# Performance work log

Hardware: AMD Instinct MI355X
Metric: run time of the kernel (lower is better)

The kernel has to match this reference:

```python
import jax, jax.numpy as jnp
import numpy as np

H = 1024      # hidden_size
MEL = 128     # mel_bins
B = 32        # batch
TENC = 512    # encoder time steps
TMEL = 400    # decoder (mel) time steps


def setup_inputs() -> dict:
    key = jax.random.key(0)
    ks = jax.random.split(key, 16)
    def w(k, shape, s=0.02):
        return jax.random.normal(k, shape, dtype=jnp.float32) * s
    return dict(
        encoder_hidden=w(ks[0], (4, B, H), 0.1),
        encoder_outputs=w(ks[1], (B, TENC, H), 0.1),
        y=w(ks[2], (B, TMEL, MEL), 1.0),
        mel_spec_lens=jax.random.randint(ks[3], (B,), 1, TMEL),
        # attention linear
        W_attn=w(ks[4], (H, H)), b_attn=jnp.zeros((H,), jnp.float32),
        # GRU layer 0 (input MEL) and layer 1 (input H); gate order r,z,n as in torch
        W_ih0=w(ks[5], (3 * H, MEL)), W_hh0=w(ks[6], (3 * H, H)),
        b_ih0=jnp.zeros((3 * H,), jnp.float32), b_hh0=jnp.zeros((3 * H,), jnp.float32),
        W_ih1=w(ks[7], (3 * H, H)), W_hh1=w(ks[8], (3 * H, H)),
        b_ih1=jnp.zeros((3 * H,), jnp.float32), b_hh1=jnp.zeros((3 * H,), jnp.float32),
        # concat2hidden, mel projection, eos gate
        Wc=w(ks[9], (H, 2 * H)), bc=jnp.zeros((H,), jnp.float32),
        Wp=w(ks[10], (MEL, H)), bp=jnp.zeros((MEL,), jnp.float32),
        Wg=w(ks[11], (1, H)), bg=jnp.zeros((1,), jnp.float32),
    )


def gru_cell(x, h, Wih, Whh, bih, bhh):
    # torch GRUCell math: gates ordered (r, z, n)
    gi = x @ Wih.T + bih          # [B, 3H]
    gh = h @ Whh.T + bhh          # [B, 3H]
    ir, iz, inn = jnp.split(gi, 3, axis=-1)
    hr, hz, hn = jnp.split(gh, 3, axis=-1)
    r = jax.nn.sigmoid(ir + hr)
    z = jax.nn.sigmoid(iz + hz)
    n = jnp.tanh(inn + r * hn)
    return (1.0 - z) * n + z * h


def reference(encoder_hidden, encoder_outputs, y, mel_spec_lens,
              W_attn, b_attn,
              W_ih0, W_hh0, b_ih0, b_hh0,
              W_ih1, W_hh1, b_ih1, b_hh1,
              Wc, bc, Wp, bp, Wg, bg):
    Bsz, Tmel, mel = y.shape
    # attention energy depends only on encoder_outputs -> hoist out of the loop (same math)
    energy = encoder_outputs @ W_attn.T + b_attn          # [B, Te, H]
    h0 = encoder_hidden[0]                                 # decoder_hidden = encoder_hidden[:num_layers]
    h1 = encoder_hidden[1]
    dec_in0 = jnp.zeros((Bsz, mel), y.dtype)               # SOS frame

    def step(carry, _):
        dec_in, h0, h1 = carry
        h0 = gru_cell(dec_in, h0, W_ih0, W_hh0, b_ih0, b_hh0)
        h1 = gru_cell(h0, h1, W_ih1, W_hh1, b_ih1, b_hh1)   # rnn_output = top-layer state [B, H]
        scores = jnp.einsum('bh,bth->bt', h1, energy)       # additive-style dot scores [B, Te]
        probs = jax.nn.softmax(scores, axis=1)
        context = jnp.einsum('bt,bth->bh', probs, encoder_outputs)  # [B, H]
        co = jnp.tanh(jnp.concatenate([h1, context], axis=-1) @ Wc.T + bc)  # [B, H]
        mel_out = co @ Wp.T + bp                            # [B, MEL]
        gate = (co @ Wg.T + bg)[:, 0]                       # [B]
        return (mel_out, h0, h1), (mel_out, gate)

    _, (mels, gates) = jax.lax.scan(step, (dec_in0, h0, h1), None, length=Tmel)
    mels = jnp.transpose(mels, (1, 0, 2))                   # [B, T, MEL]
    gates = gates.T                                          # [B, T]

    t = jnp.arange(Tmel)
    mask = t[None, :] > mel_spec_lens[:, None]               # strictly-greater, as in source
    masked_mel = jnp.where(mask[:, :, None], 0.0, mels)
    masked_gate = jnp.where(mask, 1000.0, gates)
    return masked_mel, masked_gate, mask
```

## Files before the change

### kernel.cpp

```cpp
#include <hip/hip_runtime.h>
#include <stdint.h>
#include <stddef.h>


#define TM  400

typedef unsigned short ushort_t;
typedef short  short8  __attribute__((ext_vector_type(8)));
typedef float  float4v __attribute__((ext_vector_type(4)));

#define DEVI static __device__ __forceinline__

#define SB_IH0  0
#define SB_IH1  393216
#define SB_HH0  3538944
#define SB_HH1  6684672
#define SB_AT   9830400
#define SB_WC   10878976
#define SW_TOT  12976128

__device__ __align__(16) ushort_t g_sw[SW_TOT];
__device__ __align__(16) ushort_t g_h0b[32768], g_h1b[32768];
__device__ __align__(16) float g_h0f[32768], g_h1f[32768];
__device__ __align__(16) float g_ubuf[32768], g_ctxn[32768];
__device__ __align__(16) float g_gh0[98304], g_gh1[98304];
__device__ __align__(16) float g_cbuf[32], g_sden[32];
__device__ __align__(16) float g_melsum[4096], g_gatesum[32];
__device__ __align__(16) float g_pctx[262144];
__device__ __align__(16) float g_pden[256];
__device__ __align__(16) float g_pmel[262144];
__device__ __align__(16) float g_pgate[2048];

DEVI ushort_t f2b(float f) {
  union { float f; uint32_t u; } c; c.f = f;
  uint32_t u = c.u + 0x7fffu + ((c.u >> 16) & 1u);
  return (ushort_t)(u >> 16);
}
DEVI float sigm(float x) { return 1.f / (1.f + __expf(-x)); }

DEVI float4v mfma16(short8 a, short8 b, float4v c) {
  return __builtin_amdgcn_mfma_f32_16x16x32_bf16(a, b, c, 0, 0, 0);
}

DEVI short8 frag_bias(const float* p, const float* bias) {
  short8 r;
#pragma unroll
  for (int i = 0; i < 8; ++i) r[i] = (short)f2b(p[i] + bias[i]);
  return r;
}
DEVI short8 frag_scale(const float* p, float s) {
  short8 r;
#pragma unroll
  for (int i = 0; i < 8; ++i) r[i] = (short)f2b(p[i] * s);
  return r;
}

DEVI float4v gemm_bf16(const ushort_t* Ab, int K, const ushort_t* Bw,
                       int ntile, int mu, int lane) {
  float4v acc = {0.f, 0.f, 0.f, 0.f};
  const int KB = K >> 5;
  const ushort_t* a = Ab + (size_t)(mu * 16 + (lane & 15)) * K + ((lane >> 4) << 3);
  const ushort_t* b = Bw + ((size_t)ntile * KB * 64 + lane) * 8;
  for (int kb = 0; kb < KB; ++kb) {
    short8 av = *(const short8*)(a + kb * 32);
    short8 bv = *(const short8*)(b + (size_t)kb * 512);
    acc = mfma16(av, bv, acc);
  }
  return acc;
}

DEVI float4v gemm_s1(const float* mp, const float* bp, const ushort_t* Bw,
                     int ntile, int mu, int lane) {
  float4v acc = {0.f, 0.f, 0.f, 0.f};
  const int m = mu * 16 + (lane & 15), ko = (lane >> 4) << 3;
  const ushort_t* b = Bw + ((size_t)ntile * 4 * 64 + lane) * 8;
  for (int kb = 0; kb < 4; ++kb) {
    short8 av = frag_bias(mp + m * 128 + kb * 32 + ko, bp + kb * 32 + ko);
    acc = mfma16(av, *(const short8*)(b + (size_t)kb * 512), acc);
  }
  return acc;
}

DEVI float4v gemm_s4(const ushort_t* h1b, const float* ctxn, const float* sden,
                     const ushort_t* Bw, int ntile, int mu, int lane) {
  float4v acc = {0.f, 0.f, 0.f, 0.f};
  const int m = mu * 16 + (lane & 15), ko = (lane >> 4) << 3;
  const ushort_t* a0 = h1b + m * 1024 + ko;
  const float* a1 = ctxn + m * 1024 + ko;
  const float den = sden[m];
  const float inv = (den > 1e-35f) ? (1.f / den) : 0.f;
  const ushort_t* b = Bw + ((size_t)ntile * 64 * 64 + lane) * 8;
  for (int kb = 0; kb < 32; ++kb)
    acc = mfma16(*(const short8*)(a0 + kb * 32), *(const short8*)(b + (size_t)kb * 512), acc);
  for (int kb = 32; kb < 64; ++kb) {
    short8 av = frag_scale(a1 + (kb - 32) * 32, inv);
    acc = mfma16(av, *(const short8*)(b + (size_t)kb * 512), acc);
  }
  return acc;
}

DEVI void put_tile(float* sh, int q, int lane, float4v a) {
  const int base = q * 256 + (lane & 15);
#pragma unroll
  for (int i = 0; i < 4; ++i) sh[base + ((lane >> 4) * 4 + i) * 16] = a[i];
}

__global__ void k_swz(const float* __restrict__ W0, const float* __restrict__ W1,
                      const float* __restrict__ W2, const float* __restrict__ W3,
                      const float* __restrict__ WA, const float* __restrict__ WC) {
  long fid = (long)blockIdx.x * 256 + threadIdx.x;
  if (fid >= 1622016) return;
  const float* src; int N, K; long base, local; bool tr = false;
  if      (fid < 49152)   { src = W0; N = 3072; K = 128;  base = SB_IH0; local = fid; }
  else if (fid < 442368)  { src = W1; N = 3072; K = 1024; base = SB_IH1; local = fid - 49152; }
  else if (fid < 835584)  { src = W2; N = 3072; K = 1024; base = SB_HH0; local = fid - 442368; }
  else if (fid < 1228800) { src = W3; N = 3072; K = 1024; base = SB_HH1; local = fid - 835584; }
  else if (fid < 1359872) { src = WA; N = 1024; K = 1024; base = SB_AT;  local = fid - 1228800; tr = true; }
  else                    { src = WC; N = 1024; K = 2048; base = SB_WC;  local = fid - 1359872; }
  const int L = (int)(local & 63);
  long rest = local >> 6;
  const int KB = K >> 5;
  const int kb = (int)(rest % KB);
  const int nt = (int)(rest / KB);
  const int n  = nt * 16 + (L & 15);
  const int k0 = kb * 32 + ((L >> 4) << 3);
  short8 r;
#pragma unroll
  for (int i = 0; i < 8; ++i) {
    float f = tr ? src[(size_t)(k0 + i) * N + n] : src[(size_t)n * K + (k0 + i)];
    r[i] = (short)f2b(f);
  }
  *(short8*)(g_sw + base + local * 8) = r;
}

__global__ void k_init(const float* __restrict__ ehid, const int* __restrict__ lens,
                       float* __restrict__ out, int out_size) {
  int i = blockIdx.x * 256 + threadIdx.x;
  if (i < 32768) { float v = ehid[i]; g_h0f[i] = v; g_h0b[i] = f2b(v); }
  else if (i < 65536) { int j = i - 32768; float v = ehid[32768 + j]; g_h1f[j] = v; g_h1b[j] = f2b(v); }
  else if (i < 78336) {
    int mi = i - 65536; int b = mi / 400, tt = mi % 400;
    int idx = 1651200 + mi;
    if (idx < out_size)
      out[idx] = (tt > lens[b]) ? 1.0f : 0.0f;
  }
}

__global__ void k_mel() {
  const int wg = blockIdx.x, tid = threadIdx.x;
  if (wg < 16) {
    const int e = wg * 256 + tid;
    float s = 0.f;
    for (int w = 0; w < 64; ++w) s += g_pmel[w * 4096 + e];
    g_melsum[e] = s;
  } else if (tid < 32) {
    float s = 0.f;
    for (int w = 0; w < 64; ++w) s += g_pgate[w * 32 + tid];
    g_gatesum[tid] = s;
  }
}

__global__ void k_s1(int t, const float* __restrict__ b_ih0,
                     const float* __restrict__ bp, const float* __restrict__ bg,
                     const int* __restrict__ lens,
                     float* __restrict__ out, int out_size) {
  const int wg = blockIdx.x, tid = threadIdx.x;
  const int lane = tid & 63, wv = tid >> 6;
  __shared__ __align__(16) float sh[1536];
  if (wg < 64) {
    if (t >= TM) return;
    const int qa = (wv < 2) ? wv * 2 : wv + 2;
    const int qb = (wv < 2) ? wv * 2 + 1 : -1;
    const ushort_t* SW_ih0 = g_sw + SB_IH0;
    float4v acc;
    { int g = qa >> 1, mu = qa & 1;
      acc = (t > 0) ? gemm_s1(g_melsum, bp, SW_ih0, g * 64 + wg, mu, lane)
                    : float4v{0.f, 0.f, 0.f, 0.f};
      put_tile(sh, qa, lane, acc); }
    if (qb >= 0) { int g = qb >> 1, mu = qb & 1;
      acc = (t > 0) ? gemm_s1(g_melsum, bp, SW_ih0, g * 64 + wg, mu, lane)
                    : float4v{0.f, 0.f, 0.f, 0.f};
      put_tile(sh, qb, lane, acc); }
    __syncthreads();
    const int jl = tid & 15, mr = tid >> 4, jg = wg * 16 + jl;
    const float bir = b_ih0[jg], biz = b_ih0[1024 + jg], bin = b_ih0[2048 + jg];
#pragma unroll
    for (int mu = 0; mu < 2; ++mu) {
      const int b = mu * 16 + mr;
      float gr = sh[mu * 256 + tid]       + bir + g_gh0[b * 3072 + jg];
      float gz = sh[(2 + mu) * 256 + tid] + biz + g_gh0[b * 3072 + 1024 + jg];
      float gn = sh[(4 + mu) * 256 + tid] + bin;
      float r = sigm(gr), z = sigm(gz);
      float nn = tanhf(gn + r * g_gh0[b * 3072 + 2048 + jg]);
      float h = (1.f - z) * nn + z * g_h0f[b * 1024 + jg];
      g_h0f[b * 1024 + jg] = h; g_h0b[b * 1024 + jg] = f2b(h);
    }
  } else {
    if (t == 0) return;
    const int fo = (wg - 64) * 256 + tid;
    if (fo < 4096) {
      const int b = fo >> 7, m = fo & 127;
      const bool mk = (t - 1) > lens[b];
      float v = mk ? 0.f : g_melsum[fo] + bp[m];
      int idx = b * 51200 + (t - 1) * 128 + m;
      if (idx < out_size) out[idx] = v;
    } else if (fo < 4128) {
      const int b = fo - 4096;
      const bool mk = (t - 1) > lens[b];
      float g = mk ? 1000.f : g_gatesum[b] + bg[0];
      int idx = 1638400 + b * 400 + (t - 1);
      if (idx < out_size) out[idx] = g;
    }
  }
}

__global__ void k_s2(const float* __restrict__ b_ih1) {
  const int wg = blockIdx.x, tid = threadIdx.x;
  const int lane = tid & 63, wv = tid >> 6;
  __shared__ __align__(16) float sh[1536];
  const int qa = (wv < 2) ? wv * 2 : wv + 2;
  const int qb = (wv < 2) ? wv * 2 + 1 : -1;
  const ushort_t* SW_ih1 = g_sw + SB_IH1;
  { int g = qa >> 1, mu = qa & 1;
    put_tile(sh, qa, lane, gemm_bf16(g_h0b, 1024, SW_ih1, g * 64 + wg, mu, lane)); }
  if (qb >= 0) { int g = qb >> 1, mu = qb & 1;
    put_tile(sh, qb, lane, gemm_bf16(g_h0b, 1024, SW_ih1, g * 64 + wg, mu, lane)); }
  __syncthreads();
  const int jl = tid & 15, mr = tid >> 4, jg = wg * 16 + jl;
  const float bir = b_ih1[jg], biz = b_ih1[1024 + jg], bin = b_ih1[2048 + jg];
#pragma unroll
  for (int mu = 0; mu < 2; ++mu) {
    const int b = mu * 16 + mr;
    float gr = sh[mu * 256 + tid]       + bir + g_gh1[b * 3072 + jg];
    float gz = sh[(2 + mu) * 256 + tid] + biz + g_gh1[b * 3072 + 1024 + jg];
    float gn = sh[(4 + mu) * 256 + tid] + bin;
    float r = sigm(gr), z = sigm(gz);
    float nn = tanhf(gn + r * g_gh1[b * 3072 + 2048 + jg]);
    float h = (1.f - z) * nn + z * g_h1f[b * 1024 + jg];
    g_h1f[b * 1024 + jg] = h; g_h1b[b * 1024 + jg] = f2b(h);
  }
}

__global__ void k_s2b(const float* __restrict__ b_hh0,
                      const float* __restrict__ b_hh1,
                      const float* __restrict__ b_attn) {
  const int wg = blockIdx.x, tid = threadIdx.x;
  const int lane = tid & 63, wv = tid >> 6;
  __shared__ __align__(16) float sh[1536];
  const int qa = (wv < 2) ? wv * 2 : wv + 2;
  const int qb = (wv < 2) ? wv * 2 + 1 : -1;
  if (wg < 128) {
    const ushort_t* Ab = (wg < 64) ? g_h0b : g_h1b;
    const ushort_t* Bw = g_sw + ((wg < 64) ? SB_HH0 : SB_HH1);
    const float* bhh = (wg < 64) ? b_hh0 : b_hh1;
    float* ghb = (wg < 64) ? g_gh0 : g_gh1;
    const int w16 = wg & 63;
    { int g = qa >> 1, mu = qa & 1;
      put_tile(sh, qa, lane, gemm_bf16(Ab, 1024, Bw, g * 64 + w16, mu, lane)); }
    if (qb >= 0) { int g = qb >> 1, mu = qb & 1;
      put_tile(sh, qb, lane, gemm_bf16(Ab, 1024, Bw, g * 64 + w16, mu, lane)); }
    __syncthreads();
    const int jl = tid & 15, mr = tid >> 4, jg = w16 * 16 + jl;
#pragma unroll
    for (int mu = 0; mu < 2; ++mu) {
      const int b = mu * 16 + mr;
#pragma unroll
      for (int g = 0; g < 3; ++g)
        ghb[b * 3072 + g * 1024 + jg] = sh[(g * 2 + mu) * 256 + tid] + bhh[g * 1024 + jg];
    }
  } else if (wg < 192) {
    const int nt = wg - 128;
    if (wv < 2) put_tile(sh, wv, lane, gemm_bf16(g_h1b, 1024, g_sw + SB_AT, nt, wv, lane));
    __syncthreads();
    const int nl = tid & 15, mr = tid >> 4, n = nt * 16 + nl;
    g_ubuf[mr * 1024 + n]        = sh[tid];
    g_ubuf[(16 + mr) * 1024 + n] = sh[256 + tid];
  } else {
    const int b = tid >> 3, seg = tid & 7;
    const float* hp = g_h1f + b * 1024 + seg * 128;
    const float* ba = b_attn + seg * 128;
    float s = 0.f;
    for (int k = 0; k < 128; ++k) s += hp[k] * ba[k];
    for (int off = 1; off < 8; off <<= 1) s += __shfl_xor(s, off, 64);
    if (seg == 0) g_cbuf[b] = s;
  }
}

__global__ void k_s3(const float* __restrict__ enc) {
  const int wg = blockIdx.x, tid = threadIdx.x;
  const int lane = tid & 63, wv = tid >> 6;
  __shared__ __align__(16) float sh[4160];
  const int b = wg >> 3, slot = wg & 7;
  const float* ub = g_ubuf + b * 1024;
  float4v u[4];
#pragma unroll
  for (int c = 0; c < 4; ++c) u[c] = *(const float4v*)(ub + c * 256 + lane * 4);
  const float cb = g_cbuf[b];
  float4v cx[4] = {{0.f,0.f,0.f,0.f},{0.f,0.f,0.f,0.f},{0.f,0.f,0.f,0.f},{0.f,0.f,0.f,0.f}};
  float sw = 0.f;
  const int t0 = slot * 64 + wv * 16;
  for (int it = 0; it < 16; ++it) {
    const float* encp = enc + ((size_t)(b * 512 + t0 + it) * 1024) + lane * 4;
    float4v e[4];
#pragma unroll
    for (int c = 0; c < 4; ++c) e[c] = *(const float4v*)(encp + c * 256);
    float s = 0.f;
#pragma unroll
    for (int c = 0; c < 4; ++c)
#pragma unroll
      for (int j = 0; j < 4; ++j) s += u[c][j] * e[c][j];
    for (int off = 1; off < 64; off <<= 1) s += __shfl_xor(s, off, 64);
    float sc = fminf(fmaxf(s + cb, -70.f), 70.f);
    const float p = __expf(sc);
    sw += p;
#pragma unroll
    for (int c = 0; c < 4; ++c) cx[c] += p * e[c];
  }
#pragma unroll
  for (int c = 0; c < 4; ++c)
    *(float4v*)&sh[wv * 1024 + c * 256 + lane * 4] = cx[c];
  if (lane == 0) sh[4096 + wv] = sw;
  __syncthreads();
  float4v t4 = {0.f, 0.f, 0.f, 0.f};
#pragma unroll
  for (int v = 0; v < 4; ++v) t4 += *(const float4v*)&sh[v * 1024 + tid * 4];
  *(float4v*)&g_pctx[(size_t)(slot * 32 + b) * 1024 + tid * 4] = t4;
  if (tid == 0)
    g_pden[slot * 32 + b] = sh[4096] + sh[4097] + sh[4098] + sh[4099];
}

__global__ void k_red() {
  const int b = blockIdx.x, tid = threadIdx.x;
  float4v t4 = {0.f, 0.f, 0.f, 0.f};
#pragma unroll
  for (int s = 0; s < 8; ++s)
    t4 += *(const float4v*)&g_pctx[(size_t)(s * 32 + b) * 1024 + tid * 4];
  *(float4v*)&g_ctxn[b * 1024 + tid * 4] = t4;
  if (tid == 0) {
    float d = 0.f;
#pragma unroll
    for (int s = 0; s < 8; ++s) d += g_pden[s * 32 + b];
    g_sden[b] = d;
  }
}

__global__ void k_s4(const float* __restrict__ bc, const float* __restrict__ Wp,
                     const float* __restrict__ Wg) {
  const int wg = blockIdx.x, tid = threadIdx.x;
  const int lane = tid & 63, wv = tid >> 6;
  __shared__ __align__(16) float sh[2048];
  if (wv < 2)
    put_tile(sh, wv, lane, gemm_s4(g_h1b, g_ctxn, g_sden, g_sw + SB_WC, wg, wv, lane));
  __syncthreads();
  const int jl = tid & 15, mr = tid >> 4;
  const float bcv = bc[wg * 16 + jl];
#pragma unroll
  for (int mu = 0; mu < 2; ++mu) {
    const int b = mu * 16 + mr;
    sh[1536 + b * 16 + jl] = tanhf(sh[mu * 256 + tid] + bcv);
  }
  __syncthreads();
  const int b2 = tid >> 3, mg = tid & 7;
  const float* cop = &sh[1536 + b2 * 16];
  for (int mm = 0; mm < 16; ++mm) {
    const int m = mg * 16 + mm;
    const float* wp = Wp + m * 1024 + wg * 16;
    float s = 0.f;
#pragma unroll
    for (int j2 = 0; j2 < 16; ++j2) s += wp[j2] * cop[j2];
    g_pmel[wg * 4096 + b2 * 128 + m] = s;
  }
  if (tid < 32) {
    const float* cop2 = &sh[1536 + tid * 16];
    const float* wgp = Wg + wg * 16;
    float g = 0.f;
#pragma unroll
    for (int j2 = 0; j2 < 16; ++j2) g += wgp[j2] * cop2[j2];
    g_pgate[wg * 32 + tid] = g;
  }
}

extern "C" void kernel_launch(void* const* d_in, const int* in_sizes, int n_in,
                              void* d_out, int out_size, void* d_ws, size_t ws_size,
                              hipStream_t stream) {
  const float* ehid  = (const float*)d_in[0];
  const float* enc   = (const float*)d_in[1];
  const int*   lens  = (const int*)d_in[3];
  const float* W_attn= (const float*)d_in[4];
  const float* b_attn= (const float*)d_in[5];
  const float* W_ih0 = (const float*)d_in[6];
  const float* W_hh0 = (const float*)d_in[7];
  const float* b_ih0 = (const float*)d_in[8];
  const float* b_hh0 = (const float*)d_in[9];
  const float* W_ih1 = (const float*)d_in[10];
  const float* W_hh1 = (const float*)d_in[11];
  const float* b_ih1 = (const float*)d_in[12];
  const float* b_hh1 = (const float*)d_in[13];
  const float* Wc    = (const float*)d_in[14];
  const float* bc    = (const float*)d_in[15];
  const float* Wp    = (const float*)d_in[16];
  const float* bp    = (const float*)d_in[17];
  const float* Wg    = (const float*)d_in[18];
  const float* bg    = (const float*)d_in[19];
  float* out = (float*)d_out;

  k_swz<<<6336, 256, 0, stream>>>(W_ih0, W_ih1, W_hh0, W_hh1, W_attn, Wc);
  k_init<<<306, 256, 0, stream>>>(ehid, lens, out, out_size);
  k_s2b<<<193, 256, 0, stream>>>(b_hh0, b_hh1, b_attn);
  for (int t = 0; t < TM; ++t) {
    k_mel<<<17, 256, 0, stream>>>();
    k_s1<<<96, 256, 0, stream>>>(t, b_ih0, bp, bg, lens, out, out_size);
    k_s2<<<64, 256, 0, stream>>>(b_ih1);
    k_s2b<<<193, 256, 0, stream>>>(b_hh0, b_hh1, b_attn);
    k_s3<<<256, 256, 0, stream>>>(enc);
    k_red<<<32, 256, 0, stream>>>();
    k_s4<<<64, 256, 0, stream>>>(bc, Wp, Wg);
  }
  k_mel<<<17, 256, 0, stream>>>();
  k_s1<<<96, 256, 0, stream>>>(TM, b_ih0, bp, bg, lens, out, out_size);
}
```

Before: 25.46 ms.

## Fuse decoder loop into persistent kernel with grid barriers and folded mel projection

Replaces the roughly 2800 per-step kernel launches with one persistent 256-workgroup kernel that runs all 400 timesteps, separated by software grid barriers built on atomics. It also pre-multiplies W_ih0 by Wp, so the layer-0 input GEMM reads the bf16 concat output directly and the mel reduction no longer sits on the critical path. The context partial sums now use float atomics instead of a separate reduction kernel. The risks are barrier latency, a deadlock if not all 256 workgroups are co-resident, atomic contention, and precision changes from the folded weight and nondeterministic summation order.

```diff
diff --git a/kernel.cpp b/kernel.cpp
--- a/kernel.cpp
+++ b/kernel.cpp
@@ -3,7 +3,8 @@
 #include <stddef.h>
 
 
-#define TM  400
+#define TM   400
+#define NWG  256
 
 typedef unsigned short ushort_t;
 typedef short  short8  __attribute__((ext_vector_type(8)));
@@ -11,25 +12,25 @@
 
 #define DEVI static __device__ __forceinline__
 
-#define SB_IH0  0
-#define SB_IH1  393216
-#define SB_HH0  3538944
-#define SB_HH1  6684672
-#define SB_AT   9830400
-#define SB_WC   10878976
-#define SW_TOT  12976128
+#define SB_WF   0
+#define SB_IH1  3145728
+#define SB_HH0  6291456
+#define SB_HH1  9437184
+#define SB_AT   12582912
+#define SB_WC   13631488
+#define SW_TOT  15728640
 
 __device__ __align__(16) ushort_t g_sw[SW_TOT];
+__device__ __align__(16) float    g_wf[3145728];
 __device__ __align__(16) ushort_t g_h0b[32768], g_h1b[32768];
-__device__ __align__(16) float g_h0f[32768], g_h1f[32768];
-__device__ __align__(16) float g_ubuf[32768], g_ctxn[32768];
-__device__ __align__(16) float g_gh0[98304], g_gh1[98304];
-__device__ __align__(16) float g_cbuf[32], g_sden[32];
-__device__ __align__(16) float g_melsum[4096], g_gatesum[32];
-__device__ __align__(16) float g_pctx[262144];
-__device__ __align__(16) float g_pden[256];
-__device__ __align__(16) float g_pmel[262144];
-__device__ __align__(16) float g_pgate[2048];
+__device__ __align__(16) float    g_h0f[32768], g_h1f[32768];
+__device__ __align__(16) float    g_ubuf[32768], g_cbuf[32], g_b0f[3072];
+__device__ __align__(16) float    g_gh0[98304], g_gh1[98304];
+__device__ __align__(16) float    g_ctxn[32768], g_sden[32];
+__device__ __align__(16) float    g_cof[32768];
+__device__ __align__(16) ushort_t g_cob[32768];
+__device__ __align__(64) unsigned g_bar_cnt[16];
+__device__ __align__(64) unsigned g_bar_flag[128];
 
 DEVI ushort_t f2b(float f) {
   union { float f; uint32_t u; } c; c.f = f;
@@ -42,12 +43,6 @@
   return __builtin_amdgcn_mfma_f32_16x16x32_bf16(a, b, c, 0, 0, 0);
 }
 
-DEVI short8 frag_bias(const float* p, const float* bias) {
-  short8 r;
-#pragma unroll
-  for (int i = 0; i < 8; ++i) r[i] = (short)f2b(p[i] + bias[i]);
-  return r;
-}
 DEVI short8 frag_scale(const float* p, float s) {
   short8 r;
 #pragma unroll
@@ -65,18 +60,6 @@
     short8 av = *(const short8*)(a + kb * 32);
     short8 bv = *(const short8*)(b + (size_t)kb * 512);
     acc = mfma16(av, bv, acc);
-  }
-  return acc;
-}
-
-DEVI float4v gemm_s1(const float* mp, const float* bp, const ushort_t* Bw,
-                     int ntile, int mu, int lane) {
-  float4v acc = {0.f, 0.f, 0.f, 0.f};
-  const int m = mu * 16 + (lane & 15), ko = (lane >> 4) << 3;
-  const ushort_t* b = Bw + ((size_t)ntile * 4 * 64 + lane) * 8;
-  for (int kb = 0; kb < 4; ++kb) {
-    short8 av = frag_bias(mp + m * 128 + kb * 32 + ko, bp + kb * 32 + ko);
-    acc = mfma16(av, *(const short8*)(b + (size_t)kb * 512), acc);
   }
   return acc;
 }
@@ -105,18 +88,69 @@
   for (int i = 0; i < 4; ++i) sh[base + ((lane >> 4) * 4 + i) * 16] = a[i];
 }
 
-__global__ void k_swz(const float* __restrict__ W0, const float* __restrict__ W1,
-                      const float* __restrict__ W2, const float* __restrict__ W3,
-                      const float* __restrict__ WA, const float* __restrict__ WC) {
+DEVI void gbar(unsigned idx, int tid, int wg) {
+  __syncthreads();
+  if (tid == 0) {
+    __threadfence();
+    const unsigned old = __hip_atomic_fetch_add(&g_bar_cnt[0], 1u,
+                           __ATOMIC_RELAXED, __HIP_MEMORY_SCOPE_AGENT);
+    if (old == idx * NWG - 1u) {
+#pragma unroll
+      for (int r = 0; r < 8; ++r)
+        __hip_atomic_store(&g_bar_flag[r * 16], idx,
+                           __ATOMIC_RELAXED, __HIP_MEMORY_SCOPE_AGENT);
+    } else {
+      unsigned* fp = &g_bar_flag[(wg & 7) * 16];
+      while (__hip_atomic_load(fp, __ATOMIC_RELAXED,
+                               __HIP_MEMORY_SCOPE_AGENT) < idx)
+        __builtin_amdgcn_s_sleep(4);
+    }
+    __threadfence();
+  }
+  __syncthreads();
+}
+
+__global__ void k_wf(const float* __restrict__ Wih0, const float* __restrict__ Wp) {
+  __shared__ __align__(16) float As[32][128];
+  __shared__ __align__(16) float Bs[128][64];
+  const int tid = threadIdx.x;
+  const int nt = blockIdx.x >> 4, kt = blockIdx.x & 15;
+  const int n0 = nt * 32, k0 = kt * 64;
+  {
+    const int r = tid >> 3, c0 = (tid & 7) * 16;
+    for (int i = 0; i < 16; i += 4)
+      *(float4v*)&As[r][c0 + i] = *(const float4v*)&Wih0[(size_t)(n0 + r) * 128 + c0 + i];
+  }
+  {
+    const int r = tid >> 1, c0 = (tid & 1) * 32;
+    for (int i = 0; i < 32; i += 4)
+      *(float4v*)&Bs[r][c0 + i] = *(const float4v*)&Wp[(size_t)r * 1024 + k0 + c0 + i];
+  }
+  __syncthreads();
+  const int rn = tid >> 3, kq = (tid & 7) * 8;
+  float acc[8] = {0.f, 0.f, 0.f, 0.f, 0.f, 0.f, 0.f, 0.f};
+  for (int m = 0; m < 128; ++m) {
+    const float a = As[rn][m];
+#pragma unroll
+    for (int j = 0; j < 8; ++j) acc[j] += a * Bs[m][kq + j];
+  }
+  float* dst = g_wf + (size_t)(n0 + rn) * 1024 + k0 + kq;
+#pragma unroll
+  for (int j = 0; j < 8; ++j) dst[j] = acc[j];
+}
+
+__global__ void k_swz(const float* __restrict__ W1, const float* __restrict__ W2,
+                      const float* __restrict__ W3, const float* __restrict__ WA,
+                      const float* __restrict__ WC) {
   long fid = (long)blockIdx.x * 256 + threadIdx.x;
-  if (fid >= 1622016) return;
+  if (fid >= 1966080) return;
   const float* src; int N, K; long base, local; bool tr = false;
-  if      (fid < 49152)   { src = W0; N = 3072; K = 128;  base = SB_IH0; local = fid; }
-  else if (fid < 442368)  { src = W1; N = 3072; K = 1024; base = SB_IH1; local = fid - 49152; }
-  else if (fid < 835584)  { src = W2; N = 3072; K = 1024; base = SB_HH0; local = fid - 442368; }
-  else if (fid < 1228800) { src = W3; N = 3072; K = 1024; base = SB_HH1; local = fid - 835584; }
-  else if (fid < 1359872) { src = WA; N = 1024; K = 1024; base = SB_AT;  local = fid - 1228800; tr = true; }
-  else                    { src = WC; N = 1024; K = 2048; base = SB_WC;  local = fid - 1359872; }
+  if      (fid < 393216)  { src = g_wf; N = 3072; K = 1024; base = SB_WF;  local = fid; }
+  else if (fid < 786432)  { src = W1;   N = 3072; K = 1024; base = SB_IH1; local = fid - 393216; }
+  else if (fid < 1179648) { src = W2;   N = 3072; K = 1024; base = SB_HH0; local = fid - 786432; }
+  else if (fid < 1572864) { src = W3;   N = 3072; K = 1024; base = SB_HH1; local = fid - 1179648; }
+  else if (fid < 1703936) { src = WA;   N = 1024; K = 1024; base = SB_AT;  local = fid - 1572864; tr = true; }
+  else                    { src = WC;   N = 1024; K = 2048; base = SB_WC;  local = fid - 1703936; }
   const int L = (int)(local & 63);
   long rest = local >> 6;
   const int KB = K >> 5;
@@ -134,56 +168,82 @@
 }
 
 __global__ void k_init(const float* __restrict__ ehid, const int* __restrict__ lens,
+                       const float* __restrict__ Wih0, const float* __restrict__ bp,
+                       const float* __restrict__ bih0,
                        float* __restrict__ out, int out_size) {
   int i = blockIdx.x * 256 + threadIdx.x;
+  if (i == 0) {
+    g_bar_cnt[0] = 0u;
+#pragma unroll
+    for (int r = 0; r < 8; ++r) g_bar_flag[r * 16] = 0u;
+  }
   if (i < 32768) { float v = ehid[i]; g_h0f[i] = v; g_h0b[i] = f2b(v); }
-  else if (i < 65536) { int j = i - 32768; float v = ehid[32768 + j]; g_h1f[j] = v; g_h1b[j] = f2b(v); }
-  else if (i < 78336) {
+  else if (i < 65536) {
+    int j = i - 32768; float v = ehid[32768 + j];
+    g_h1f[j] = v; g_h1b[j] = f2b(v);
+  } else if (i < 78336) {
     int mi = i - 65536; int b = mi / 400, tt = mi % 400;
     int idx = 1651200 + mi;
-    if (idx < out_size)
-      out[idx] = (tt > lens[b]) ? 1.0f : 0.0f;
-  }
-}
-
-__global__ void k_mel() {
-  const int wg = blockIdx.x, tid = threadIdx.x;
-  if (wg < 16) {
-    const int e = wg * 256 + tid;
-    float s = 0.f;
-    for (int w = 0; w < 64; ++w) s += g_pmel[w * 4096 + e];
-    g_melsum[e] = s;
-  } else if (tid < 32) {
-    float s = 0.f;
-    for (int w = 0; w < 64; ++w) s += g_pgate[w * 32 + tid];
-    g_gatesum[tid] = s;
-  }
-}
-
-__global__ void k_s1(int t, const float* __restrict__ b_ih0,
-                     const float* __restrict__ bp, const float* __restrict__ bg,
-                     const int* __restrict__ lens,
-                     float* __restrict__ out, int out_size) {
+    if (idx < out_size) out[idx] = (tt > lens[b]) ? 1.0f : 0.0f;
+  } else if (i < 81408) {
+    int n = i - 78336;
+    float s = bih0[n];
+    const float* wr = Wih0 + (size_t)n * 128;
+    for (int m = 0; m < 128; ++m) s += bp[m] * wr[m];
+    g_b0f[n] = s;
+  }
+}
+
+__global__ void k_pre(const float* __restrict__ b_hh0, const float* __restrict__ b_hh1) {
   const int wg = blockIdx.x, tid = threadIdx.x;
   const int lane = tid & 63, wv = tid >> 6;
   __shared__ __align__(16) float sh[1536];
+  const int qa = (wv < 2) ? wv * 2 : wv + 2;
+  const int qb = (wv < 2) ? wv * 2 + 1 : -1;
+  const ushort_t* Ab = (wg < 64) ? g_h0b : g_h1b;
+  const ushort_t* Bw = g_sw + ((wg < 64) ? SB_HH0 : SB_HH1);
+  const float* bhh = (wg < 64) ? b_hh0 : b_hh1;
+  float* ghb = (wg < 64) ? g_gh0 : g_gh1;
+  const int w16 = wg & 63;
+  { int g = qa >> 1, mu = qa & 1;
+    put_tile(sh, qa, lane, gemm_bf16(Ab, 1024, Bw, g * 64 + w16, mu, lane)); }
+  if (qb >= 0) { int g = qb >> 1, mu = qb & 1;
+    put_tile(sh, qb, lane, gemm_bf16(Ab, 1024, Bw, g * 64 + w16, mu, lane)); }
+  __syncthreads();
+  const int jl = tid & 15, mr = tid >> 4, jg = w16 * 16 + jl;
+#pragma unroll
+  for (int mu = 0; mu < 2; ++mu) {
+    const int b = mu * 16 + mr;
+#pragma unroll
+    for (int g = 0; g < 3; ++g)
+      ghb[b * 3072 + g * 1024 + jg] = sh[(g * 2 + mu) * 256 + tid] + bhh[g * 1024 + jg];
+  }
+}
+
+DEVI void phaseA(int t, int wg, int tid,
+                 const float* __restrict__ b_ih0, const float* __restrict__ bp,
+                 const float* __restrict__ Wp, const float* __restrict__ Wg,
+                 const float* __restrict__ bg, const int* __restrict__ lens,
+                 float* __restrict__ out, int out_size, float* sh) {
+  const int lane = tid & 63, wv = tid >> 6;
   if (wg < 64) {
     if (t >= TM) return;
     const int qa = (wv < 2) ? wv * 2 : wv + 2;
     const int qb = (wv < 2) ? wv * 2 + 1 : -1;
-    const ushort_t* SW_ih0 = g_sw + SB_IH0;
+    const ushort_t* SW = g_sw + SB_WF;
     float4v acc;
     { int g = qa >> 1, mu = qa & 1;
-      acc = (t > 0) ? gemm_s1(g_melsum, bp, SW_ih0, g * 64 + wg, mu, lane)
+      acc = (t > 0) ? gemm_bf16(g_cob, 1024, SW, g * 64 + wg, mu, lane)
                     : float4v{0.f, 0.f, 0.f, 0.f};
       put_tile(sh, qa, lane, acc); }
     if (qb >= 0) { int g = qb >> 1, mu = qb & 1;
-      acc = (t > 0) ? gemm_s1(g_melsum, bp, SW_ih0, g * 64 + wg, mu, lane)
+      acc = (t > 0) ? gemm_bf16(g_cob, 1024, SW, g * 64 + wg, mu, lane)
                     : float4v{0.f, 0.f, 0.f, 0.f};
       put_tile(sh, qb, lane, acc); }
     __syncthreads();
     const int jl = tid & 15, mr = tid >> 4, jg = wg * 16 + jl;
-    const float bir = b_ih0[jg], biz = b_ih0[1024 + jg], bin = b_ih0[2048 + jg];
+    const float* bs = (t > 0) ? g_b0f : b_ih0;
+    const float bir = bs[jg], biz = bs[1024 + jg], bin = bs[2048 + jg];
 #pragma unroll
     for (int mu = 0; mu < 2; ++mu) {
       const int b = mu * 16 + mr;
@@ -195,70 +255,88 @@
       float h = (1.f - z) * nn + z * g_h0f[b * 1024 + jg];
       g_h0f[b * 1024 + jg] = h; g_h0b[b * 1024 + jg] = f2b(h);
     }
-  } else {
+  } else if (wg < 128) {
     if (t == 0) return;
-    const int fo = (wg - 64) * 256 + tid;
-    if (fo < 4096) {
-      const int b = fo >> 7, m = fo & 127;
+    const int idx = wg - 64, b = idx & 31, mh = idx >> 5;
+    const int m = mh * 64 + (tid >> 2), q = tid & 3;
+    const float* cop = g_cof + b * 1024 + q * 256;
+    const float* wpp = Wp + (size_t)m * 1024 + q * 256;
+    float s = 0.f;
+#pragma unroll 8
+    for (int k = 0; k < 256; k += 4) {
+      float4v cv = *(const float4v*)(cop + k);
+      float4v wv4 = *(const float4v*)(wpp + k);
+      s += cv[0] * wv4[0] + cv[1] * wv4[1] + cv[2] * wv4[2] + cv[3] * wv4[3];
+    }
+    s += __shfl_xor(s, 1, 64);
+    s += __shfl_xor(s, 2, 64);
+    if (q == 0) {
       const bool mk = (t - 1) > lens[b];
-      float v = mk ? 0.f : g_melsum[fo] + bp[m];
-      int idx = b * 51200 + (t - 1) * 128 + m;
-      if (idx < out_size) out[idx] = v;
-    } else if (fo < 4128) {
-      const int b = fo - 4096;
+      const float v = mk ? 0.f : (s + bp[m]);
+      const int oidx = b * 51200 + (t - 1) * 128 + m;
+      if (oidx < out_size) out[oidx] = v;
+    }
+  } else if (wg == 128) {
+    if (t == 0) return;
+    const int b = tid >> 3, seg = tid & 7;
+    const float* cop = g_cof + b * 1024 + seg * 128;
+    const float* wgp = Wg + seg * 128;
+    float s = 0.f;
+#pragma unroll 8
+    for (int k = 0; k < 128; k += 4) {
+      float4v cv = *(const float4v*)(cop + k);
+      float4v wv4 = *(const float4v*)(wgp + k);
+      s += cv[0] * wv4[0] + cv[1] * wv4[1] + cv[2] * wv4[2] + cv[3] * wv4[3];
+    }
+    for (int off = 1; off < 8; off <<= 1) s += __shfl_xor(s, off, 64);
+    if (seg == 0) {
       const bool mk = (t - 1) > lens[b];
-      float g = mk ? 1000.f : g_gatesum[b] + bg[0];
-      int idx = 1638400 + b * 400 + (t - 1);
-      if (idx < out_size) out[idx] = g;
-    }
-  }
-}
-
-__global__ void k_s2(const float* __restrict__ b_ih1) {
-  const int wg = blockIdx.x, tid = threadIdx.x;
+      const float g = mk ? 1000.f : (s + bg[0]);
+      const int oidx = 1638400 + b * 400 + (t - 1);
+      if (oidx < out_size) out[oidx] = g;
+    }
+  } else if (wg >= 129 && wg < 137) {
+    const int z = (wg - 129) * 256 + tid;
+    float4v* c4 = (float4v*)g_ctxn;
+    const float4v zv = {0.f, 0.f, 0.f, 0.f};
+#pragma unroll
+    for (int r = 0; r < 4; ++r) c4[z + r * 2048] = zv;
+    if (wg == 129 && tid < 32) g_sden[tid] = 0.f;
+  }
+}
+
+DEVI void phaseB(int wg, int tid, const float* __restrict__ b_ih1,
+                 const float* __restrict__ b_hh0, float* sh) {
   const int lane = tid & 63, wv = tid >> 6;
-  __shared__ __align__(16) float sh[1536];
   const int qa = (wv < 2) ? wv * 2 : wv + 2;
   const int qb = (wv < 2) ? wv * 2 + 1 : -1;
-  const ushort_t* SW_ih1 = g_sw + SB_IH1;
-  { int g = qa >> 1, mu = qa & 1;
-    put_tile(sh, qa, lane, gemm_bf16(g_h0b, 1024, SW_ih1, g * 64 + wg, mu, lane)); }
-  if (qb >= 0) { int g = qb >> 1, mu = qb & 1;
-    put_tile(sh, qb, lane, gemm_bf16(g_h0b, 1024, SW_ih1, g * 64 + wg, mu, lane)); }
-  __syncthreads();
-  const int jl = tid & 15, mr = tid >> 4, jg = wg * 16 + jl;
-  const float bir = b_ih1[jg], biz = b_ih1[1024 + jg], bin = b_ih1[2048 + jg];
-#pragma unroll
-  for (int mu = 0; mu < 2; ++mu) {
-    const int b = mu * 16 + mr;
-    float gr = sh[mu * 256 + tid]       + bir + g_gh1[b * 3072 + jg];
-    float gz = sh[(2 + mu) * 256 + tid] + biz + g_gh1[b * 3072 + 1024 + jg];
-    float gn = sh[(4 + mu) * 256 + tid] + bin;
-    float r = sigm(gr), z = sigm(gz);
-    float nn = tanhf(gn + r * g_gh1[b * 3072 + 2048 + jg]);
-    float h = (1.f - z) * nn + z * g_h1f[b * 1024 + jg];
-    g_h1f[b * 1024 + jg] = h; g_h1b[b * 1024 + jg] = f2b(h);
-  }
-}
-
-__global__ void k_s2b(const float* __restrict__ b_hh0,
-                      const float* __restrict__ b_hh1,
-                      const float* __restrict__ b_attn) {
-  const int wg = blockIdx.x, tid = threadIdx.x;
-  const int lane = tid & 63, wv = tid >> 6;
-  __shared__ __align__(16) float sh[1536];
-  const int qa = (wv < 2) ? wv * 2 : wv + 2;
-  const int qb = (wv < 2) ? wv * 2 + 1 : -1;
-  if (wg < 128) {
-    const ushort_t* Ab = (wg < 64) ? g_h0b : g_h1b;
-    const ushort_t* Bw = g_sw + ((wg < 64) ? SB_HH0 : SB_HH1);
-    const float* bhh = (wg < 64) ? b_hh0 : b_hh1;
-    float* ghb = (wg < 64) ? g_gh0 : g_gh1;
-    const int w16 = wg & 63;
+  if (wg < 64) {
+    const ushort_t* SW = g_sw + SB_IH1;
     { int g = qa >> 1, mu = qa & 1;
-      put_tile(sh, qa, lane, gemm_bf16(Ab, 1024, Bw, g * 64 + w16, mu, lane)); }
+      put_tile(sh, qa, lane, gemm_bf16(g_h0b, 1024, SW, g * 64 + wg, mu, lane)); }
     if (qb >= 0) { int g = qb >> 1, mu = qb & 1;
-      put_tile(sh, qb, lane, gemm_bf16(Ab, 1024, Bw, g * 64 + w16, mu, lane)); }
+      put_tile(sh, qb, lane, gemm_bf16(g_h0b, 1024, SW, g * 64 + wg, mu, lane)); }
+    __syncthreads();
+    const int jl = tid & 15, mr = tid >> 4, jg = wg * 16 + jl;
+    const float bir = b_ih1[jg], biz = b_ih1[1024 + jg], bin = b_ih1[2048 + jg];
+#pragma unroll
+    for (int mu = 0; mu < 2; ++mu) {
+      const int b = mu * 16 + mr;
+      float gr = sh[mu * 256 + tid]       + bir + g_gh1[b * 3072 + jg];
+      float gz = sh[(2 + mu) * 256 + tid] + biz + g_gh1[b * 3072 + 1024 + jg];
+      float gn = sh[(4 + mu) * 256 + tid] + bin;
+      float r = sigm(gr), z = sigm(gz);
+      float nn = tanhf(gn + r * g_gh1[b * 3072 + 2048 + jg]);
+      float h = (1.f - z) * nn + z * g_h1f[b * 1024 + jg];
+      g_h1f[b * 1024 + jg] = h; g_h1b[b * 1024 + jg] = f2b(h);
+    }
+  } else if (wg < 128) {
+    const int w16 = wg - 64;
+    const ushort_t* SW = g_sw + SB_HH0;
+    { int g = qa >> 1, mu = qa & 1;
+      put_tile(sh, qa, lane, gemm_bf16(g_h0b, 1024, SW, g * 64 + w16, mu, lane)); }
+    if (qb >= 0) { int g = qb >> 1, mu = qb & 1;
+      put_tile(sh, qb, lane, gemm_bf16(g_h0b, 1024, SW, g * 64 + w16, mu, lane)); }
     __syncthreads();
     const int jl = tid & 15, mr = tid >> 4, jg = w16 * 16 + jl;
 #pragma unroll
@@ -266,16 +344,39 @@
       const int b = mu * 16 + mr;
 #pragma unroll
       for (int g = 0; g < 3; ++g)
-        ghb[b * 3072 + g * 1024 + jg] = sh[(g * 2 + mu) * 256 + tid] + bhh[g * 1024 + jg];
-    }
-  } else if (wg < 192) {
-    const int nt = wg - 128;
+        g_gh0[b * 3072 + g * 1024 + jg] = sh[(g * 2 + mu) * 256 + tid] + b_hh0[g * 1024 + jg];
+    }
+  }
+}
+
+DEVI void phaseC(int wg, int tid, const float* __restrict__ b_hh1,
+                 const float* __restrict__ b_attn, float* sh) {
+  const int lane = tid & 63, wv = tid >> 6;
+  if (wg < 64) {
+    const int qa = (wv < 2) ? wv * 2 : wv + 2;
+    const int qb = (wv < 2) ? wv * 2 + 1 : -1;
+    const ushort_t* SW = g_sw + SB_HH1;
+    { int g = qa >> 1, mu = qa & 1;
+      put_tile(sh, qa, lane, gemm_bf16(g_h1b, 1024, SW, g * 64 + wg, mu, lane)); }
+    if (qb >= 0) { int g = qb >> 1, mu = qb & 1;
+      put_tile(sh, qb, lane, gemm_bf16(g_h1b, 1024, SW, g * 64 + wg, mu, lane)); }
+    __syncthreads();
+    const int jl = tid & 15, mr = tid >> 4, jg = wg * 16 + jl;
+#pragma unroll
+    for (int mu = 0; mu < 2; ++mu) {
+      const int b = mu * 16 + mr;
+#pragma unroll
+      for (int g = 0; g < 3; ++g)
+        g_gh1[b * 3072 + g * 1024 + jg] = sh[(g * 2 + mu) * 256 + tid] + b_hh1[g * 1024 + jg];
+    }
+  } else if (wg < 128) {
+    const int nt = wg - 64;
     if (wv < 2) put_tile(sh, wv, lane, gemm_bf16(g_h1b, 1024, g_sw + SB_AT, nt, wv, lane));
     __syncthreads();
     const int nl = tid & 15, mr = tid >> 4, n = nt * 16 + nl;
     g_ubuf[mr * 1024 + n]        = sh[tid];
     g_ubuf[(16 + mr) * 1024 + n] = sh[256 + tid];
-  } else {
+  } else if (wg == 128) {
     const int b = tid >> 3, seg = tid & 7;
     const float* hp = g_h1f + b * 1024 + seg * 128;
     const float* ba = b_attn + seg * 128;
@@ -286,10 +387,8 @@
   }
 }
 
-__global__ void k_s3(const float* __restrict__ enc) {
-  const int wg = blockIdx.x, tid = threadIdx.x;
+DEVI void phaseD(int wg, int tid, const float* __restrict__ enc, float* sh) {
   const int lane = tid & 63, wv = tid >> 6;
-  __shared__ __align__(16) float sh[4160];
   const int b = wg >> 3, slot = wg & 7;
   const float* ub = g_ubuf + b * 1024;
   float4v u[4];
@@ -323,32 +422,17 @@
   __syncthreads();
   float4v t4 = {0.f, 0.f, 0.f, 0.f};
 #pragma unroll
-  for (int v = 0; v < 4; ++v) t4 += *(const float4v*)&sh[v * 1024 + tid * 4];
-  *(float4v*)&g_pctx[(size_t)(slot * 32 + b) * 1024 + tid * 4] = t4;
+  for (int vv = 0; vv < 4; ++vv) t4 += *(const float4v*)&sh[vv * 1024 + tid * 4];
+  float* dst = g_ctxn + b * 1024 + tid * 4;
+#pragma unroll
+  for (int c = 0; c < 4; ++c) unsafeAtomicAdd(dst + c, t4[c]);
   if (tid == 0)
-    g_pden[slot * 32 + b] = sh[4096] + sh[4097] + sh[4098] + sh[4099];
-}
-
-__global__ void k_red() {
-  const int b = blockIdx.x, tid = threadIdx.x;
-  float4v t4 = {0.f, 0.f, 0.f, 0.f};
-#pragma unroll
-  for (int s = 0; s < 8; ++s)
-    t4 += *(const float4v*)&g_pctx[(size_t)(s * 32 + b) * 1024 + tid * 4];
-  *(float4v*)&g_ctxn[b * 1024 + tid * 4] = t4;
-  if (tid == 0) {
-    float d = 0.f;
-#pragma unroll
-    for (int s = 0; s < 8; ++s) d += g_pden[s * 32 + b];
-    g_sden[b] = d;
-  }
-}
-
-__global__ void k_s4(const float* __restrict__ bc, const float* __restrict__ Wp,
-                     const float* __restrict__ Wg) {
-  const int wg = blockIdx.x, tid = threadIdx.x;
+    unsafeAtomicAdd(&g_sden[b], sh[4096] + sh[4097] + sh[4098] + sh[4099]);
+}
+
+DEVI void phaseE(int wg, int tid, const float* __restrict__ bc, float* sh) {
+  if (wg >= 64) return;
   const int lane = tid & 63, wv = tid >> 6;
-  __shared__ __align__(16) float sh[2048];
   if (wv < 2)
     put_tile(sh, wv, lane, gemm_s4(g_h1b, g_ctxn, g_sden, g_sw + SB_WC, wg, wv, lane));
   __syncthreads();
@@ -357,27 +441,36 @@
 #pragma unroll
   for (int mu = 0; mu < 2; ++mu) {
     const int b = mu * 16 + mr;
-    sh[1536 + b * 16 + jl] = tanhf(sh[mu * 256 + tid] + bcv);
-  }
-  __syncthreads();
-  const int b2 = tid >> 3, mg = tid & 7;
-  const float* cop = &sh[1536 + b2 * 16];
-  for (int mm = 0; mm < 16; ++mm) {
-    const int m = mg * 16 + mm;
-    const float* wp = Wp + m * 1024 + wg * 16;
-    float s = 0.f;
-#pragma unroll
-    for (int j2 = 0; j2 < 16; ++j2) s += wp[j2] * cop[j2];
-    g_pmel[wg * 4096 + b2 * 128 + m] = s;
-  }
-  if (tid < 32) {
-    const float* cop2 = &sh[1536 + tid * 16];
-    const float* wgp = Wg + wg * 16;
-    float g = 0.f;
-#pragma unroll
-    for (int j2 = 0; j2 < 16; ++j2) g += wgp[j2] * cop2[j2];
-    g_pgate[wg * 32 + tid] = g;
-  }
+    const float v = tanhf(sh[mu * 256 + tid] + bcv);
+    g_cof[b * 1024 + wg * 16 + jl] = v;
+    g_cob[b * 1024 + wg * 16 + jl] = f2b(v);
+  }
+}
+
+__global__ void __launch_bounds__(256) k_run(
+    const float* __restrict__ enc,
+    const float* __restrict__ b_ih0, const float* __restrict__ b_ih1,
+    const float* __restrict__ b_hh0, const float* __restrict__ b_hh1,
+    const float* __restrict__ b_attn, const float* __restrict__ bc,
+    const float* __restrict__ Wp, const float* __restrict__ bp,
+    const float* __restrict__ Wg, const float* __restrict__ bg,
+    const int* __restrict__ lens, float* __restrict__ out, int out_size) {
+  __shared__ __align__(16) float sh[4160];
+  const int wg = blockIdx.x, tid = threadIdx.x;
+  unsigned bar = 0;
+  for (int t = 0; t < TM; ++t) {
+    phaseA(t, wg, tid, b_ih0, bp, Wp, Wg, bg, lens, out, out_size, sh);
+    gbar(++bar, tid, wg);
+    phaseB(wg, tid, b_ih1, b_hh0, sh);
+    gbar(++bar, tid, wg);
+    phaseC(wg, tid, b_hh1, b_attn, sh);
+    gbar(++bar, tid, wg);
+    phaseD(wg, tid, enc, sh);
+    gbar(++bar, tid, wg);
+    phaseE(wg, tid, bc, sh);
+    gbar(++bar, tid, wg);
+  }
+  phaseA(TM, wg, tid, b_ih0, bp, Wp, Wg, bg, lens, out, out_size, sh);
 }
 
 extern "C" void kernel_launch(void* const* d_in, const int* in_sizes, int n_in,
@@ -404,18 +497,10 @@
   const float* bg    = (const float*)d_in[19];
   float* out = (float*)d_out;
 
-  k_swz<<<6336, 256, 0, stream>>>(W_ih0, W_ih1, W_hh0, W_hh1, W_attn, Wc);
-  k_init<<<306, 256, 0, stream>>>(ehid, lens, out, out_size);
-  k_s2b<<<193, 256, 0, stream>>>(b_hh0, b_hh1, b_attn);
-  for (int t = 0; t < TM; ++t) {
-    k_mel<<<17, 256, 0, stream>>>();
-    k_s1<<<96, 256, 0, stream>>>(t, b_ih0, bp, bg, lens, out, out_size);
-    k_s2<<<64, 256, 0, stream>>>(b_ih1);
-    k_s2b<<<193, 256, 0, stream>>>(b_hh0, b_hh1, b_attn);
-    k_s3<<<256, 256, 0, stream>>>(enc);
-    k_red<<<32, 256, 0, stream>>>();
-    k_s4<<<64, 256, 0, stream>>>(bc, Wp, Wg);
-  }
-  k_mel<<<17, 256, 0, stream>>>();
-  k_s1<<<96, 256, 0, stream>>>(TM, b_ih0, bp, bg, lens, out, out_size);
-}
+  k_wf  <<<1536, 256, 0, stream>>>(W_ih0, Wp);
+  k_swz <<<7680, 256, 0, stream>>>(W_ih1, W_hh0, W_hh1, W_attn, Wc);
+  k_init<<<318, 256, 0, stream>>>(ehid, lens, W_ih0, bp, b_ih0, out, out_size);
+  k_pre <<<128, 256, 0, stream>>>(b_hh0, b_hh1);
+  k_run <<<NWG, 256, 0, stream>>>(enc, b_ih0, b_ih1, b_hh0, b_hh1, b_attn, bc,
+                                  Wp, bp, Wg, bg, lens, out, out_size);
+}
```

Result: slower. 69.04 ms (+171.2%).
